# Kernel optimization log

Measured on AMD Instinct MI355X. Metric: run time of the kernel, lower is better.

## Reference

```python
import jax, jax.numpy as jnp
import numpy as np

N = 100000   # nodes
E = 3200000  # edges (before self-loops)
H = 16       # hidden_dim
G = 1000     # graphs in batch
NEG_SLOPE = 0.2


def setup_inputs() -> dict:
    key = jax.random.key(0)
    ks = jax.random.split(key, 40)
    rn = lambda k, s: (jax.random.normal(k, s, jnp.float32) * 0.1)
    inp = {}
    inp['x'] = jax.random.normal(ks[0], (N, 1), jnp.float32)
    inp['edge_index'] = jax.random.randint(ks[1], (2, E), 0, N, jnp.int64)
    inp['batch'] = jnp.sort(jax.random.randint(ks[2], (N,), 0, G, jnp.int64))
    dims = [1, H, H]
    i = 3
    for l in range(3):
        d = dims[l]
        inp[f'c{l}_Wl'] = rn(ks[i], (d, H)); i += 1
        inp[f'c{l}_bl'] = jnp.zeros((H,), jnp.float32)
        inp[f'c{l}_Wr'] = rn(ks[i], (d, H)); i += 1
        inp[f'c{l}_br'] = jnp.zeros((H,), jnp.float32)
        inp[f'c{l}_att'] = rn(ks[i], (H,)); i += 1
        inp[f'c{l}_bias'] = jnp.zeros((H,), jnp.float32)
        inp[f'l{l}_W'] = rn(ks[i], (H, H)); i += 1
        inp[f'l{l}_b'] = jnp.zeros((H,), jnp.float32)
    for j, (a, b) in enumerate([(H, H), (H, H), (H, 1)]):
        inp[f'o{j}_W'] = rn(ks[i], (a, b)); i += 1
        inp[f'o{j}_b'] = jnp.zeros((b,), jnp.float32)
    return inp


def gatv2_conv(x, src, dst, Wl, bl, Wr, br, att, bias):
    # PyG GATv2Conv, heads=1: x_j = lin_l(x)[src], x_i = lin_r(x)[dst]
    xl = x @ Wl + bl  # [N,H] source transform
    xr = x @ Wr + br  # [N,H] target transform
    e = jax.nn.leaky_relu(xl[src] + xr[dst], NEG_SLOPE)  # [E+N,H]
    score = e @ att  # [E+N]
    # scatter-softmax over incoming edges of each destination node
    m = jax.ops.segment_max(score, dst, num_segments=N)
    ex = jnp.exp(score - m[dst])
    denom = jax.ops.segment_sum(ex, dst, num_segments=N)
    alpha = ex / denom[dst]
    out = jax.ops.segment_sum(alpha[:, None] * xl[src], dst, num_segments=N)
    return out + bias


def reference(x, c0_Wl, c0_bl, c0_Wr, c0_br, c0_att, c0_bias,
              c1_Wl, c1_bl, c1_Wr, c1_br, c1_att, c1_bias,
              c2_Wl, c2_bl, c2_Wr, c2_br, c2_att, c2_bias,
              l0_W, l0_b, l1_W, l1_b, l2_W, l2_b,
              o0_W, o0_b, o1_W, o1_b, o2_W, o2_b,
              edge_index, batch):
    # add self-loops (PyG GATv2Conv default add_self_loops=True)
    loops = jnp.arange(N, dtype=edge_index.dtype)
    ei = jnp.concatenate([edge_index, jnp.stack([loops, loops])], axis=1)
    src, dst = ei[0], ei[1]
    convs = [(c0_Wl, c0_bl, c0_Wr, c0_br, c0_att, c0_bias),
             (c1_Wl, c1_bl, c1_Wr, c1_br, c1_att, c1_bias),
             (c2_Wl, c2_bl, c2_Wr, c2_br, c2_att, c2_bias)]
    lins = [(l0_W, l0_b), (l1_W, l1_b), (l2_W, l2_b)]
    h = x
    for (Wl, bl, Wr, br, att, bias), (W, b) in zip(convs, lins):
        h = jax.nn.relu(gatv2_conv(h, src, dst, Wl, bl, Wr, br, att, bias))
        h = h @ W + b
    g = jax.ops.segment_sum(h, batch, num_segments=G)  # global_add_pool -> [G,H]
    g = jax.nn.relu(g @ o0_W + o0_b)
    g = jax.nn.relu(g @ o1_W + o1_b)
    return g @ o2_W + o2_b  # [G,1]
```

## Files before the change

### kernel.cpp

```cpp
#include <hip/hip_runtime.h>
#include <hip/hip_fp16.h>

#define HD 16

static constexpr int NN = 100000;
static constexpr int EE = 3200000;
static constexpr int GG = 1000;
static constexpr int ET = EE + NN;
static constexpr float NEG = 0.2f;
static constexpr float LOG2E = 1.44269504f;

static constexpr int BSH = 8;
static constexpr int NB = (NN + 255) >> BSH;
static constexpr int EPB = 8192;
static constexpr int GB = (ET + EPB - 1) / EPB;
static constexpr int ITER = EPB / 1024;

__device__ __forceinline__ int imin(int a, int b) { return a < b ? a : b; }

template <int N>
__device__ __forceinline__ float row_ror_add(float v) {
  int m = __builtin_amdgcn_update_dpp(0, __float_as_int(v), 0x120 + N, 0xF, 0xF, true);
  return v + __int_as_float(m);
}
__device__ __forceinline__ float row_sum16(float v) {
  v = row_ror_add<1>(v);
  v = row_ror_add<2>(v);
  v = row_ror_add<4>(v);
  v = row_ror_add<8>(v);
  return v;
}

__global__ void k_chist(const int* __restrict__ edst, int* __restrict__ chist) {
  __shared__ int sh[NB];
  int t = threadIdx.x;
  for (int i = t; i < NB; i += 1024) sh[i] = 0;
  __syncthreads();
  int b0 = blockIdx.x * EPB;
#pragma unroll
  for (int i = 0; i < ITER; ++i) {
    int e = b0 + t + i * 1024;
    if (e < ET) {
      int d = (e < EE) ? edst[e] : e - EE;
      atomicAdd(&sh[d >> BSH], 1);
    }
  }
  __syncthreads();
  for (int i = t; i < NB; i += 1024)
    if (sh[i]) atomicAdd(&chist[i], sh[i]);
}

__global__ void k_cscan(const int* __restrict__ chist, int* __restrict__ cbase,
                        int* __restrict__ ccur, int* __restrict__ rowptr) {
  __shared__ int sh[512];
  int t = threadIdx.x;
  sh[t] = (t < NB) ? chist[t] : 0;
  __syncthreads();
  for (int off = 1; off < 512; off <<= 1) {
    int v = sh[t];
    int a = (t >= off) ? sh[t - off] : 0;
    __syncthreads();
    sh[t] = v + a;
    __syncthreads();
  }
  if (t < NB) {
    int b = (t == 0) ? 0 : sh[t - 1];
    cbase[t] = b;
    ccur[t] = b;
  }
  if (t == 0) rowptr[NN] = ET;
}

__global__ void k_csplit(const int* __restrict__ esrc, const int* __restrict__ edst,
                         int* __restrict__ ccur, unsigned* __restrict__ tmp) {
  __shared__ int hist[NB];
  __shared__ int base[NB];
  int t = threadIdx.x;
  for (int i = t; i < NB; i += 1024) hist[i] = 0;
  __syncthreads();
  int b0 = blockIdx.x * EPB;
  int sl[ITER], dl[ITER];
#pragma unroll
  for (int i = 0; i < ITER; ++i) {
    int e = b0 + t + i * 1024;
    int s = -1, d = 0;
    if (e < ET) {
      if (e < EE) { s = esrc[e]; d = edst[e]; } else { s = e - EE; d = s; }
      atomicAdd(&hist[d >> BSH], 1);
    }
    sl[i] = s; dl[i] = d;
  }
  __syncthreads();
  for (int i = t; i < NB; i += 1024) {
    int c = hist[i];
    base[i] = c ? atomicAdd(&ccur[i], c) : 0;
    hist[i] = 0;
  }
  __syncthreads();
#pragma unroll
  for (int i = 0; i < ITER; ++i) {
    int s = sl[i];
    if (s >= 0) {
      int d = dl[i], bb = d >> BSH;
      int slot = base[bb] + atomicAdd(&hist[bb], 1);
      tmp[slot] = ((unsigned)(d & 255) << 17) | (unsigned)s;
    }
  }
}

__global__ void k_fsort(const unsigned* __restrict__ tmp, const int* __restrict__ cbase,
                        const int* __restrict__ chist, int* __restrict__ rowptr,
                        int* __restrict__ psrc) {
  __shared__ int fh[256];
  __shared__ int fs[256];
  int b = blockIdx.x, t = threadIdx.x;
  if (t < 256) fh[t] = 0;
  __syncthreads();
  int beg = cbase[b], cnt = chist[b];
  for (int i = t; i < cnt; i += 1024)
    atomicAdd(&fh[tmp[beg + i] >> 17], 1);
  __syncthreads();
  if (t < 256) fs[t] = fh[t];
  __syncthreads();
  for (int off = 1; off < 256; off <<= 1) {
    int v = 0, a = 0;
    if (t < 256) { v = fs[t]; if (t >= off) a = fs[t - off]; }
    __syncthreads();
    if (t < 256) fs[t] = v + a;
    __syncthreads();
  }
  if (t < 256) {
    int ex = fs[t] - fh[t];
    fs[t] = ex;
    int node = (b << BSH) + t;
    if (node < NN) rowptr[node] = beg + ex;
  }
  __syncthreads();
  for (int i = t; i < cnt; i += 1024) {
    unsigned v = tmp[beg + i];
    int ld = v >> 17;
    psrc[beg + atomicAdd(&fs[ld], 1)] = (int)(v & 0x1FFFFu);
  }
}

__global__ void k_comb(const float* __restrict__ W0, const float* __restrict__ b0,
                       const float* __restrict__ Wl1, const float* __restrict__ bl1,
                       const float* __restrict__ Wr1, const float* __restrict__ br1,
                       const float* __restrict__ W1, const float* __restrict__ b1,
                       const float* __restrict__ Wl2, const float* __restrict__ bl2,
                       const float* __restrict__ Wr2, const float* __restrict__ br2,
                       float* __restrict__ Wc0l, float* __restrict__ bc0l,
                       float* __restrict__ Wc0r, float* __restrict__ bc0r,
                       float* __restrict__ Wc1l, float* __restrict__ bc1l,
                       float* __restrict__ Wc1r, float* __restrict__ bc1r) {
  const float *W, *b, *P, *bp;
  float *Wo, *bo;
  switch (blockIdx.x) {
    case 0:  W = W0; b = b0; P = Wl1; bp = bl1; Wo = Wc0l; bo = bc0l; break;
    case 1:  W = W0; b = b0; P = Wr1; bp = br1; Wo = Wc0r; bo = bc0r; break;
    case 2:  W = W1; b = b1; P = Wl2; bp = bl2; Wo = Wc1l; bo = bc1l; break;
    default: W = W1; b = b1; P = Wr2; bp = br2; Wo = Wc1r; bo = bc1r; break;
  }
  int t = threadIdx.x;
  int c = t >> 4, k = t & 15;
  float s = 0.f;
#pragma unroll
  for (int i = 0; i < 16; ++i) s = fmaf(W[c * 16 + i], P[i * 16 + k], s);
  Wo[t] = s;
  if (t < 16) {
    float sb = bp[t];
#pragma unroll
    for (int i = 0; i < 16; ++i) sb = fmaf(b[i], P[i * 16 + t], sb);
    bo[t] = sb;
  }
}

template <int MODE>
__global__ void k_conv(const int* __restrict__ rowptr, const int* __restrict__ psrc,
                       const float* __restrict__ x,
                       const float* __restrict__ Wl0, const float* __restrict__ bl0,
                       const float* __restrict__ Wr0, const float* __restrict__ br0,
                       const __half* __restrict__ xlh, const float* __restrict__ xr,
                       const float* __restrict__ att, const float* __restrict__ cbias,
                       const float* __restrict__ Wcl, const float* __restrict__ bcl,
                       const float* __restrict__ Wcr, const float* __restrict__ bcr,
                       const float* __restrict__ Wlast, const float* __restrict__ blast,
                       __half* __restrict__ oxlh, float* __restrict__ oxr,
                       float* __restrict__ gpool, const int* __restrict__ batch) {
  int gt = blockIdx.x * blockDim.x + threadIdx.x;
  int n = gt >> 6;
  if (n >= NN) return;
  int lane = threadIdx.x & 63;
  int sub = lane >> 4;
  int k = lane & (HD - 1);
  float attk2 = att[k] * LOG2E;
  float wl0k, bl0k, xrk;
  if constexpr (MODE == 0) {
    wl0k = Wl0[k]; bl0k = bl0[k];
    xrk = fmaf(x[n], Wr0[k], br0[k]);
  } else {
    xrk = xr[(size_t)n * HD + k];
  }
  int beg = rowptr[n], end = rowptr[n + 1];
  int e1 = end - 1;
  int p = beg + sub;
  int i0 = psrc[imin(p, e1)];
  int i1 = psrc[imin(p + 4, e1)];
  int i2 = psrc[imin(p + 8, e1)];
  int i3 = psrc[imin(p + 12, e1)];
  float l0 = 0.f, l1 = 0.f, l2 = 0.f, l3 = 0.f;
  float a0 = 0.f, a1 = 0.f, a2 = 0.f, a3 = 0.f;
  for (; p < end; p += 16) {
    int j0 = psrc[imin(p + 16, e1)];
    int j1 = psrc[imin(p + 20, e1)];
    int j2 = psrc[imin(p + 24, e1)];
    int j3 = psrc[imin(p + 28, e1)];
    float x0, x1, x2, x3;
    if constexpr (MODE == 0) {
      x0 = fmaf(x[i0], wl0k, bl0k);
      x1 = fmaf(x[i1], wl0k, bl0k);
      x2 = fmaf(x[i2], wl0k, bl0k);
      x3 = fmaf(x[i3], wl0k, bl0k);
    } else {
      x0 = __half2float(xlh[(size_t)i0 * HD + k]);
      x1 = __half2float(xlh[(size_t)i1 * HD + k]);
      x2 = __half2float(xlh[(size_t)i2 * HD + k]);
      x3 = __half2float(xlh[(size_t)i3 * HD + k]);
    }
    float u0 = x0 + xrk; u0 = fmaxf(u0, NEG * u0);
    float u1 = x1 + xrk; u1 = fmaxf(u1, NEG * u1);
    float u2 = x2 + xrk; u2 = fmaxf(u2, NEG * u2);
    float u3 = x3 + xrk; u3 = fmaxf(u3, NEG * u3);
    float sc0 = row_sum16(u0 * attk2);
    float sc1 = row_sum16(u1 * attk2);
    float sc2 = row_sum16(u2 * attk2);
    float sc3 = row_sum16(u3 * attk2);
    float pe0 = __builtin_amdgcn_exp2f(sc0);
    float pe1 = (p + 4 < end) ? __builtin_amdgcn_exp2f(sc1) : 0.f;
    float pe2 = (p + 8 < end) ? __builtin_amdgcn_exp2f(sc2) : 0.f;
    float pe3 = (p + 12 < end) ? __builtin_amdgcn_exp2f(sc3) : 0.f;
    l0 += pe0; a0 = fmaf(pe0, x0, a0);
    l1 += pe1; a1 = fmaf(pe1, x1, a1);
    l2 += pe2; a2 = fmaf(pe2, x2, a2);
    l3 += pe3; a3 = fmaf(pe3, x3, a3);
    i0 = j0; i1 = j1; i2 = j2; i3 = j3;
  }
  float l = (l0 + l1) + (l2 + l3);
  float acc = (a0 + a1) + (a2 + a3);
  l += __shfl_xor(l, 16, 64);
  l += __shfl_xor(l, 32, 64);
  acc += __shfl_xor(acc, 16, 64);
  acc += __shfl_xor(acc, 32, 64);
  float hk = fmaf(acc, __builtin_amdgcn_rcpf(l), cbias[k]);
  hk = fmaxf(hk, 0.f);
  if constexpr (MODE == 2) {
    float o = 0.f;
#pragma unroll
    for (int i = 0; i < 4; ++i) {
      int c = 4 * sub + i;
      float hc = __shfl(hk, c, 16);
      o = fmaf(hc, Wlast[c * HD + k], o);
    }
    o += __shfl_xor(o, 16, 64);
    o += __shfl_xor(o, 32, 64);
    if (sub == 0) atomicAdd(gpool + (size_t)batch[n] * HD + k, o + blast[k]);
  } else {
    const float* Wsel = (sub < 2) ? Wcl : Wcr;
    int cb = (sub & 1) * 8;
    float o = 0.f;
#pragma unroll
    for (int i = 0; i < 8; ++i) {
      int c = cb + i;
      float hc = __shfl(hk, c, 16);
      o = fmaf(hc, Wsel[c * HD + k], o);
    }
    o += __shfl_xor(o, 16, 64);
    if (sub == 0) oxlh[(size_t)n * HD + k] = __float2half(o + bcl[k]);
    else if (sub == 2) oxr[(size_t)n * HD + k] = o + bcr[k];
  }
}

__global__ void k_mlp(const float* __restrict__ g,
                      const float* __restrict__ W0, const float* __restrict__ b0,
                      const float* __restrict__ W1, const float* __restrict__ b1,
                      const float* __restrict__ W2, const float* __restrict__ b2,
                      float* __restrict__ out) {
  int gi = blockIdx.x * blockDim.x + threadIdx.x;
  if (gi >= GG) return;
  float v[HD], a[HD];
  const float4* g4 = reinterpret_cast<const float4*>(g + (size_t)gi * HD);
#pragma unroll
  for (int i = 0; i < 4; ++i) {
    float4 tv = g4[i];
    v[4 * i] = tv.x; v[4 * i + 1] = tv.y; v[4 * i + 2] = tv.z; v[4 * i + 3] = tv.w;
  }
#pragma unroll
  for (int j = 0; j < HD; ++j) {
    float s = b0[j];
#pragma unroll
    for (int kk = 0; kk < HD; ++kk) s = fmaf(v[kk], W0[kk * HD + j], s);
    a[j] = s > 0.f ? s : 0.f;
  }
#pragma unroll
  for (int j = 0; j < HD; ++j) {
    float s = b1[j];
#pragma unroll
    for (int kk = 0; kk < HD; ++kk) s = fmaf(a[kk], W1[kk * HD + j], s);
    v[j] = s > 0.f ? s : 0.f;
  }
  float s = b2[0];
#pragma unroll
  for (int kk = 0; kk < HD; ++kk) s = fmaf(v[kk], W2[kk], s);
  out[gi] = s;
}

extern "C" void kernel_launch(void* const* d_in, const int* in_sizes, int n_in,
                              void* d_out, int out_size, void* d_ws, size_t ws_size,
                              hipStream_t stream) {
  const float* x = (const float*)d_in[0];
  const int* ei = (const int*)d_in[1];
  const int* batch = (const int*)d_in[2];
  const int* esrc = ei;
  const int* edst = ei + EE;

  const float* cW[3][6];
  const float* lW[3][2];
  int i = 3;
  for (int l = 0; l < 3; ++l) {
    for (int j = 0; j < 6; ++j) cW[l][j] = (const float*)d_in[i++];
    lW[l][0] = (const float*)d_in[i++];
    lW[l][1] = (const float*)d_in[i++];
  }
  const float *oW[3], *ob[3];
  for (int j = 0; j < 3; ++j) {
    oW[j] = (const float*)d_in[i++];
    ob[j] = (const float*)d_in[i++];
  }

  char* ws = (char*)d_ws;
  size_t off = 0;
  auto alloc = [&](size_t bytes) {
    void* p = ws + off;
    off = (off + bytes + 255) & ~(size_t)255;
    return p;
  };
  int* psrc = (int*)alloc((size_t)ET * 4);
  int* rowptr = (int*)alloc((size_t)(NN + 1) * 4);
  int* chist = (int*)alloc((size_t)NB * 4);
  int* cbase = (int*)alloc((size_t)NB * 4);
  int* ccur = (int*)alloc((size_t)NB * 4);
  float* Wc0l = (float*)alloc(256 * 4);
  float* Wc0r = (float*)alloc(256 * 4);
  float* Wc1l = (float*)alloc(256 * 4);
  float* Wc1r = (float*)alloc(256 * 4);
  float* bc0l = (float*)alloc(16 * 4);
  float* bc0r = (float*)alloc(16 * 4);
  float* bc1l = (float*)alloc(16 * 4);
  float* bc1r = (float*)alloc(16 * 4);
  size_t NNHD = (size_t)NN * HD;
  size_t featBytes = NNHD * 12 + (size_t)GG * HD * 4;
  size_t uniBytes = (size_t)ET * 4 > featBytes ? (size_t)ET * 4 : featBytes;
  char* uni = (char*)alloc(uniBytes);
  unsigned* tmp = (unsigned*)uni;
  __half* xlhB = (__half*)uni;
  float* xrB = (float*)(uni + NNHD * 2);
  __half* xlhA = (__half*)(uni + NNHD * 6);
  float* xrA = (float*)(uni + NNHD * 8);
  float* gbuf = (float*)(uni + NNHD * 12);

  const int B = 256;
  const int gConv = (NN * 64 + B - 1) / B;
  const int gMlp = (GG + B - 1) / B;

  hipMemsetAsync(chist, 0, (size_t)NB * 4, stream);

  k_comb<<<4, 256, 0, stream>>>(lW[0][0], lW[0][1],
                                cW[1][0], cW[1][1], cW[1][2], cW[1][3],
                                lW[1][0], lW[1][1],
                                cW[2][0], cW[2][1], cW[2][2], cW[2][3],
                                Wc0l, bc0l, Wc0r, bc0r, Wc1l, bc1l, Wc1r, bc1r);

  k_chist<<<GB, 1024, 0, stream>>>(edst, chist);
  k_cscan<<<1, 512, 0, stream>>>(chist, cbase, ccur, rowptr);
  k_csplit<<<GB, 1024, 0, stream>>>(esrc, edst, ccur, tmp);
  k_fsort<<<NB, 1024, 0, stream>>>(tmp, cbase, chist, rowptr, psrc);

  hipMemsetAsync(gbuf, 0, (size_t)GG * HD * 4, stream);

  k_conv<0><<<gConv, B, 0, stream>>>(rowptr, psrc, x,
                                     cW[0][0], cW[0][1], cW[0][2], cW[0][3],
                                     nullptr, nullptr, cW[0][4], cW[0][5],
                                     Wc0l, bc0l, Wc0r, bc0r, nullptr, nullptr,
                                     xlhB, xrB, nullptr, nullptr);
  k_conv<1><<<gConv, B, 0, stream>>>(rowptr, psrc, nullptr,
                                     nullptr, nullptr, nullptr, nullptr,
                                     xlhB, xrB, cW[1][4], cW[1][5],
                                     Wc1l, bc1l, Wc1r, bc1r, nullptr, nullptr,
                                     xlhA, xrA, nullptr, nullptr);
  k_conv<2><<<gConv, B, 0, stream>>>(rowptr, psrc, nullptr,
                                     nullptr, nullptr, nullptr, nullptr,
                                     xlhA, xrA, cW[2][4], cW[2][5],
                                     nullptr, nullptr, nullptr, nullptr,
                                     lW[2][0], lW[2][1],
                                     nullptr, nullptr, gbuf, batch);

  k_mlp<<<gMlp, B, 0, stream>>>(gbuf, oW[0], ob[0], oW[1], ob[1], oW[2], ob[2],
                                (float*)d_out);
}
```

Measured before the change: 256.4 us.

## Remap conv lanes to four features per lane with quad DPP reductions

The edge-attention loop changes lane mapping. Each wavefront now covers 16 edges at a time, and each lane handles 4 features loaded as a vector, instead of 4 edges with one feature per lane. The score reduction becomes a 2-step quad DPP sum instead of a 4-step row sum, and gathers become 8-byte vector loads. This cuts reduction instructions and gather count per edge. In exchange it needs a longer shuffle reduction at the end and a shared-memory round trip to restore the per-feature layout for the projection epilogue.

```diff
diff --git a/kernel.cpp b/kernel.cpp
--- a/kernel.cpp
+++ b/kernel.cpp
@@ -18,17 +18,16 @@
 
 __device__ __forceinline__ int imin(int a, int b) { return a < b ? a : b; }
 
-template <int N>
-__device__ __forceinline__ float row_ror_add(float v) {
-  int m = __builtin_amdgcn_update_dpp(0, __float_as_int(v), 0x120 + N, 0xF, 0xF, true);
-  return v + __int_as_float(m);
-}
-__device__ __forceinline__ float row_sum16(float v) {
-  v = row_ror_add<1>(v);
-  v = row_ror_add<2>(v);
-  v = row_ror_add<4>(v);
-  v = row_ror_add<8>(v);
-  return v;
+__device__ __forceinline__ float h2f(unsigned short u) {
+  __half_raw r; r.x = u;
+  return __half2float((__half)r);
+}
+
+__device__ __forceinline__ float quad_sum(float v) {
+  int a = __builtin_amdgcn_update_dpp(0, __float_as_int(v), 0xB1, 0xF, 0xF, true);
+  v += __int_as_float(a);
+  int b = __builtin_amdgcn_update_dpp(0, __float_as_int(v), 0x4E, 0xF, 0xF, true);
+  return v + __int_as_float(b);
 }
 
 __global__ void k_chist(const int* __restrict__ edst, int* __restrict__ chist) {
@@ -187,72 +186,97 @@
                        const float* __restrict__ Wlast, const float* __restrict__ blast,
                        __half* __restrict__ oxlh, float* __restrict__ oxr,
                        float* __restrict__ gpool, const int* __restrict__ batch) {
+  __shared__ float hsh[4][16];
   int gt = blockIdx.x * blockDim.x + threadIdx.x;
   int n = gt >> 6;
   if (n >= NN) return;
   int lane = threadIdx.x & 63;
-  int sub = lane >> 4;
-  int k = lane & (HD - 1);
-  float attk2 = att[k] * LOG2E;
-  float wl0k, bl0k, xrk;
+  int q = lane & 3;
+  int ei = lane >> 2;
+  int k0 = q * 4;
+  float4 att4 = *reinterpret_cast<const float4*>(att + k0);
+  att4.x *= LOG2E; att4.y *= LOG2E; att4.z *= LOG2E; att4.w *= LOG2E;
+  float4 xr4, wl4, bl4;
   if constexpr (MODE == 0) {
-    wl0k = Wl0[k]; bl0k = bl0[k];
-    xrk = fmaf(x[n], Wr0[k], br0[k]);
+    wl4 = *reinterpret_cast<const float4*>(Wl0 + k0);
+    bl4 = *reinterpret_cast<const float4*>(bl0 + k0);
+    float4 wr4 = *reinterpret_cast<const float4*>(Wr0 + k0);
+    float4 br4 = *reinterpret_cast<const float4*>(br0 + k0);
+    float xn = x[n];
+    xr4.x = fmaf(xn, wr4.x, br4.x);
+    xr4.y = fmaf(xn, wr4.y, br4.y);
+    xr4.z = fmaf(xn, wr4.z, br4.z);
+    xr4.w = fmaf(xn, wr4.w, br4.w);
   } else {
-    xrk = xr[(size_t)n * HD + k];
+    xr4 = *reinterpret_cast<const float4*>(xr + (size_t)n * HD + k0);
   }
   int beg = rowptr[n], end = rowptr[n + 1];
   int e1 = end - 1;
-  int p = beg + sub;
-  int i0 = psrc[imin(p, e1)];
-  int i1 = psrc[imin(p + 4, e1)];
-  int i2 = psrc[imin(p + 8, e1)];
-  int i3 = psrc[imin(p + 12, e1)];
-  float l0 = 0.f, l1 = 0.f, l2 = 0.f, l3 = 0.f;
-  float a0 = 0.f, a1 = 0.f, a2 = 0.f, a3 = 0.f;
-  for (; p < end; p += 16) {
-    int j0 = psrc[imin(p + 16, e1)];
-    int j1 = psrc[imin(p + 20, e1)];
-    int j2 = psrc[imin(p + 24, e1)];
-    int j3 = psrc[imin(p + 28, e1)];
-    float x0, x1, x2, x3;
+  int p = beg + ei;
+  int s0 = psrc[imin(p, e1)];
+  int s1 = psrc[imin(p + 16, e1)];
+  float l0 = 0.f, l1 = 0.f;
+  float a00 = 0.f, a01 = 0.f, a02 = 0.f, a03 = 0.f;
+  float a10 = 0.f, a11 = 0.f, a12 = 0.f, a13 = 0.f;
+  for (; p < end; p += 32) {
+    int t0 = psrc[imin(p + 32, e1)];
+    int t1 = psrc[imin(p + 48, e1)];
+    float x00, x01, x02, x03, x10, x11, x12, x13;
     if constexpr (MODE == 0) {
-      x0 = fmaf(x[i0], wl0k, bl0k);
-      x1 = fmaf(x[i1], wl0k, bl0k);
-      x2 = fmaf(x[i2], wl0k, bl0k);
-      x3 = fmaf(x[i3], wl0k, bl0k);
+      float xs0 = x[s0], xs1 = x[s1];
+      x00 = fmaf(xs0, wl4.x, bl4.x); x01 = fmaf(xs0, wl4.y, bl4.y);
+      x02 = fmaf(xs0, wl4.z, bl4.z); x03 = fmaf(xs0, wl4.w, bl4.w);
+      x10 = fmaf(xs1, wl4.x, bl4.x); x11 = fmaf(xs1, wl4.y, bl4.y);
+      x12 = fmaf(xs1, wl4.z, bl4.z); x13 = fmaf(xs1, wl4.w, bl4.w);
     } else {
-      x0 = __half2float(xlh[(size_t)i0 * HD + k]);
-      x1 = __half2float(xlh[(size_t)i1 * HD + k]);
-      x2 = __half2float(xlh[(size_t)i2 * HD + k]);
-      x3 = __half2float(xlh[(size_t)i3 * HD + k]);
-    }
-    float u0 = x0 + xrk; u0 = fmaxf(u0, NEG * u0);
-    float u1 = x1 + xrk; u1 = fmaxf(u1, NEG * u1);
-    float u2 = x2 + xrk; u2 = fmaxf(u2, NEG * u2);
-    float u3 = x3 + xrk; u3 = fmaxf(u3, NEG * u3);
-    float sc0 = row_sum16(u0 * attk2);
-    float sc1 = row_sum16(u1 * attk2);
-    float sc2 = row_sum16(u2 * attk2);
-    float sc3 = row_sum16(u3 * attk2);
+      ushort4 r0 = *reinterpret_cast<const ushort4*>(xlh + (size_t)s0 * HD + k0);
+      ushort4 r1 = *reinterpret_cast<const ushort4*>(xlh + (size_t)s1 * HD + k0);
+      x00 = h2f(r0.x); x01 = h2f(r0.y); x02 = h2f(r0.z); x03 = h2f(r0.w);
+      x10 = h2f(r1.x); x11 = h2f(r1.y); x12 = h2f(r1.z); x13 = h2f(r1.w);
+    }
+    float u, sp0 = 0.f, sp1 = 0.f;
+    u = x00 + xr4.x; u = fmaxf(u, NEG * u); sp0 = fmaf(u, att4.x, sp0);
+    u = x01 + xr4.y; u = fmaxf(u, NEG * u); sp0 = fmaf(u, att4.y, sp0);
+    u = x02 + xr4.z; u = fmaxf(u, NEG * u); sp0 = fmaf(u, att4.z, sp0);
+    u = x03 + xr4.w; u = fmaxf(u, NEG * u); sp0 = fmaf(u, att4.w, sp0);
+    u = x10 + xr4.x; u = fmaxf(u, NEG * u); sp1 = fmaf(u, att4.x, sp1);
+    u = x11 + xr4.y; u = fmaxf(u, NEG * u); sp1 = fmaf(u, att4.y, sp1);
+    u = x12 + xr4.z; u = fmaxf(u, NEG * u); sp1 = fmaf(u, att4.z, sp1);
+    u = x13 + xr4.w; u = fmaxf(u, NEG * u); sp1 = fmaf(u, att4.w, sp1);
+    float sc0 = quad_sum(sp0);
+    float sc1 = quad_sum(sp1);
     float pe0 = __builtin_amdgcn_exp2f(sc0);
-    float pe1 = (p + 4 < end) ? __builtin_amdgcn_exp2f(sc1) : 0.f;
-    float pe2 = (p + 8 < end) ? __builtin_amdgcn_exp2f(sc2) : 0.f;
-    float pe3 = (p + 12 < end) ? __builtin_amdgcn_exp2f(sc3) : 0.f;
-    l0 += pe0; a0 = fmaf(pe0, x0, a0);
-    l1 += pe1; a1 = fmaf(pe1, x1, a1);
-    l2 += pe2; a2 = fmaf(pe2, x2, a2);
-    l3 += pe3; a3 = fmaf(pe3, x3, a3);
-    i0 = j0; i1 = j1; i2 = j2; i3 = j3;
-  }
-  float l = (l0 + l1) + (l2 + l3);
-  float acc = (a0 + a1) + (a2 + a3);
-  l += __shfl_xor(l, 16, 64);
-  l += __shfl_xor(l, 32, 64);
-  acc += __shfl_xor(acc, 16, 64);
-  acc += __shfl_xor(acc, 32, 64);
-  float hk = fmaf(acc, __builtin_amdgcn_rcpf(l), cbias[k]);
-  hk = fmaxf(hk, 0.f);
+    float pe1 = (p + 16 < end) ? __builtin_amdgcn_exp2f(sc1) : 0.f;
+    l0 += pe0;
+    a00 = fmaf(pe0, x00, a00); a01 = fmaf(pe0, x01, a01);
+    a02 = fmaf(pe0, x02, a02); a03 = fmaf(pe0, x03, a03);
+    l1 += pe1;
+    a10 = fmaf(pe1, x10, a10); a11 = fmaf(pe1, x11, a11);
+    a12 = fmaf(pe1, x12, a12); a13 = fmaf(pe1, x13, a13);
+    s0 = t0; s1 = t1;
+  }
+  float l = l0 + l1;
+  float b0 = a00 + a10, b1 = a01 + a11, b2 = a02 + a12, b3 = a03 + a13;
+#pragma unroll
+  for (int st = 4; st <= 32; st <<= 1) {
+    l += __shfl_xor(l, st, 64);
+    b0 += __shfl_xor(b0, st, 64);
+    b1 += __shfl_xor(b1, st, 64);
+    b2 += __shfl_xor(b2, st, 64);
+    b3 += __shfl_xor(b3, st, 64);
+  }
+  float rl = __builtin_amdgcn_rcpf(l);
+  float4 cb4 = *reinterpret_cast<const float4*>(cbias + k0);
+  float h0 = fmaxf(fmaf(b0, rl, cb4.x), 0.f);
+  float h1 = fmaxf(fmaf(b1, rl, cb4.y), 0.f);
+  float h2 = fmaxf(fmaf(b2, rl, cb4.z), 0.f);
+  float h3 = fmaxf(fmaf(b3, rl, cb4.w), 0.f);
+  int w = threadIdx.x >> 6;
+  if (lane < 4)
+    *reinterpret_cast<float4*>(&hsh[w][lane * 4]) = make_float4(h0, h1, h2, h3);
+  int sub = lane >> 4;
+  int k = lane & 15;
+  float hk = hsh[w][k];
   if constexpr (MODE == 2) {
     float o = 0.f;
 #pragma unroll
```

Measured after the change: 245.7 us. 1.04x faster.
